# Performance work log

Hardware: AMD Instinct MI355X
Metric: run time of the kernel (lower is better)

Reference implementation:

```python
import jax, jax.numpy as jnp
import numpy as np
from jax.ops import segment_sum

NUM_NODES = 50000
IN_DIM = 512
OUT_DIM = 512
NNZ = 150000
NUM_EDGES = 10000


def setup_inputs() -> dict:
    key = jax.random.key(0)
    k1, k2, k3, k4, k5 = jax.random.split(key, 5)
    X = jax.random.normal(k1, (NUM_NODES, IN_DIM), dtype=jnp.float32)
    V = jax.random.randint(k2, (NNZ,), 0, NUM_NODES)
    E = jax.random.randint(k3, (NNZ,), 0, NUM_EDGES)
    # Linear(in_dim, out_dim) params (torch default init ~ U(-1/sqrt(in), 1/sqrt(in)))
    bound = 1.0 / np.sqrt(IN_DIM)
    W = jax.random.uniform(k4, (OUT_DIM, IN_DIM), minval=-bound, maxval=bound, dtype=jnp.float32)
    b = jax.random.uniform(k5, (OUT_DIM,), minval=-bound, maxval=bound, dtype=jnp.float32)
    eps = jnp.float32(0.1)
    return {"X": X, "V": V, "E": E, "num_edges": NUM_EDGES, "W": W, "b": b, "eps": eps}


def reference(X, V, E, num_edges, W, b, eps):
    num_nodes = X.shape[0]
    # Stage 1: node -> hyperedge (mean of member node features)
    gathered = X[V]  # (nnz, in_dim)
    edge_sum = segment_sum(gathered, E, num_segments=num_edges)          # (num_edges, in_dim)
    count = segment_sum(jnp.ones((E.shape[0],), X.dtype), E, num_segments=num_edges)
    edge_emb = edge_sum / jnp.clip(count, 1.0)[:, None]
    # Stage 2: hyperedge -> node (sum of incident hyperedge embeddings)
    node_msg = segment_sum(edge_emb[E], V, num_segments=num_nodes)       # (num_nodes, in_dim)
    # GIN self-loop + linear
    h = (1.0 + eps) * X + node_msg
    return h @ W.T + b
```

## Files before the change

kernel.cpp:

```cpp
#include <hip/hip_runtime.h>

#define D     512
#define NEDGE 10000
#define ECAP  48
#define NCAP  24
#define CPAD  32

typedef __attribute__((ext_vector_type(8))) short  bf16x8;
typedef __attribute__((ext_vector_type(4))) float  f32x4;
typedef __attribute__((ext_vector_type(8))) unsigned short u16x8;

static __device__ __forceinline__ unsigned short f2bf(float f) {
    union { float f; unsigned u; } c; c.f = f;
    unsigned u = c.u;
    return (unsigned short)((u + 0x7FFFu + ((u >> 16) & 1u)) >> 16);
}
static __device__ __forceinline__ float bf2f(unsigned short s) {
    union { unsigned u; float f; } c; c.u = ((unsigned)s) << 16; return c.f;
}

__global__ __launch_bounds__(256)
void prep(const int* __restrict__ V, const int* __restrict__ E,
          const float* __restrict__ W, const float* __restrict__ X,
          int* __restrict__ ecnt, int* __restrict__ ncnt,
          int* __restrict__ emem, int* __restrict__ nmem,
          unsigned short* __restrict__ wb, unsigned short* __restrict__ xb,
          int nnz, int xgroups)
{
    const int i = blockIdx.x * 256 + threadIdx.x;
    if (i < nnz) {
        const int e = E[i], v = V[i];
        const int p = atomicAdd(&ecnt[(size_t)e * CPAD], 1);
        if (p < ECAP) emem[e * ECAP + p] = v;
        const int q = atomicAdd(&ncnt[(size_t)v * CPAD], 1);
        if (q < NCAP) nmem[v * NCAP + q] = e;
    }
    if (i < xgroups) {
        const float4 a = *(reinterpret_cast<const float4*>(X) + i);
        ushort4 o;
        o.x = f2bf(a.x); o.y = f2bf(a.y); o.z = f2bf(a.z); o.w = f2bf(a.w);
        *(reinterpret_cast<ushort4*>(xb) + i) = o;
    }
    if (i < D * D / 4) {
        const float4 a = *(reinterpret_cast<const float4*>(W) + i);
        ushort4 o;
        o.x = f2bf(a.x); o.y = f2bf(a.y); o.z = f2bf(a.z); o.w = f2bf(a.w);
        *(reinterpret_cast<ushort4*>(wb) + i) = o;
    }
}

__global__ __launch_bounds__(256, 5)
void gemm_y(const unsigned short* __restrict__ xb, const unsigned short* __restrict__ wb,
            unsigned short* __restrict__ y, int M, int q, int r)
{
    __shared__ unsigned short S[2 * 128 * 64];
    unsigned short* As = S;
    unsigned short* Bs = S + 128 * 64;

    const int orig = blockIdx.x;
    const int xcd = orig & 7, lin = orig >> 3;
    const int wg = (xcd < r ? xcd * (q + 1) : r * (q + 1) + (xcd - r) * q) + lin;
    const int row0 = (wg >> 2) * 128;
    const int col0 = (wg & 3) * 128;

    const int tid  = threadIdx.x;
    const int lane = tid & 63;
    const int wave = tid >> 6;
    const int wr = wave >> 1, wc = wave & 1;

    const int l15   = lane & 15;
    const int khalf = lane >> 4;
    const int crow  = lane >> 3;
    const int slot  = lane & 7;

    f32x4 acc[4][4] = {};

    for (int t = 0; t < 8; ++t) {
        const int k0 = t * 64;
        #pragma unroll
        for (int cc = 0; cc < 8; ++cc) {
            const int chunk = wave * 8 + cc;
            const unsigned short* src; unsigned short* dst; int c, base;
            if (chunk < 16) { c = chunk;      src = xb; base = row0; dst = As; }
            else            { c = chunk - 16; src = wb; base = col0; dst = Bs; }
            const int rr = c * 8 + crow;
            const int gslot = slot ^ (rr & 7);
            const unsigned short* gp = src + (size_t)(base + rr) * D + k0 + gslot * 8;
            unsigned short* lp = dst + c * 512;
            __builtin_amdgcn_global_load_lds(
                (const __attribute__((address_space(1))) void*)gp,
                (__attribute__((address_space(3))) void*)lp, 16, 0, 0);
        }
        asm volatile("s_waitcnt vmcnt(0)" ::: "memory");
        __syncthreads();

        #pragma unroll
        for (int s = 0; s < 2; ++s) {
            bf16x8 a[4], b[4];
            #pragma unroll
            for (int i = 0; i < 4; ++i) {
                const int rr = wr * 64 + i * 16 + l15;
                const int sl = (khalf | (s << 2)) ^ (rr & 7);
                a[i] = *reinterpret_cast<const bf16x8*>(As + rr * 64 + sl * 8);
            }
            #pragma unroll
            for (int j = 0; j < 4; ++j) {
                const int rr = wc * 64 + j * 16 + l15;
                const int sl = (khalf | (s << 2)) ^ (rr & 7);
                b[j] = *reinterpret_cast<const bf16x8*>(Bs + rr * 64 + sl * 8);
            }
            #pragma unroll
            for (int i = 0; i < 4; ++i)
                #pragma unroll
                for (int j = 0; j < 4; ++j)
                    acc[i][j] = __builtin_amdgcn_mfma_f32_16x16x32_bf16(a[i], b[j], acc[i][j], 0, 0, 0);
        }
        __syncthreads();
    }

    const int row4 = (lane >> 4) * 4;
    #pragma unroll
    for (int j = 0; j < 4; ++j) {
        const int lc = wc * 64 + j * 16 + l15;
        #pragma unroll
        for (int i = 0; i < 4; ++i) {
            #pragma unroll
            for (int reg = 0; reg < 4; ++reg) {
                const int lr = wr * 64 + i * 16 + row4 + reg;
                const float own = acc[i][j][reg];
                const float nb  = __shfl_xor(own, 1);
                if (!(lane & 1)) {
                    const unsigned dw = (unsigned)f2bf(own) | ((unsigned)f2bf(nb) << 16);
                    *reinterpret_cast<unsigned*>(S + lr * 128 + lc) = dw;
                }
            }
        }
    }
    __syncthreads();
    #pragma unroll
    for (int k = 0; k < 8; ++k) {
        const int lr  = k * 16 + (tid >> 4);
        const int lc8 = (tid & 15) * 8;
        const int gr  = row0 + lr;
        if (gr < M) {
            const u16x8 vv = *reinterpret_cast<const u16x8*>(S + lr * 128 + lc8);
            *reinterpret_cast<u16x8*>(y + (size_t)gr * D + col0 + lc8) = vv;
        }
    }
}

__global__ __launch_bounds__(256)
void edge_gather(const unsigned short* __restrict__ y, const int* __restrict__ ecnt,
                 const int* __restrict__ emem, unsigned short* __restrict__ ey)
{
    __shared__ float red[D];
    const int e = blockIdx.x;
    const int t = threadIdx.x;
    const int half = t >> 7;
    const int l = t & 127;
    int deg = ecnt[(size_t)e * CPAD]; if (deg > ECAP) deg = ECAP;
    const int* lst = emem + e * ECAP;
    float4 acc = make_float4(0.f, 0.f, 0.f, 0.f);
    for (int m = half; m < deg; m += 2) {
        const int v = lst[m];
        const ushort4 x = *reinterpret_cast<const ushort4*>(y + (size_t)v * D + l * 4);
        acc.x += bf2f(x.x); acc.y += bf2f(x.y);
        acc.z += bf2f(x.z); acc.w += bf2f(x.w);
    }
    if (half) *reinterpret_cast<float4*>(red + l * 4) = acc;
    __syncthreads();
    if (!half) {
        const float4 o = *reinterpret_cast<const float4*>(red + l * 4);
        const float inv = 1.0f / fmaxf((float)deg, 1.0f);
        ushort4 r;
        r.x = f2bf((acc.x + o.x) * inv);
        r.y = f2bf((acc.y + o.y) * inv);
        r.z = f2bf((acc.z + o.z) * inv);
        r.w = f2bf((acc.w + o.w) * inv);
        *reinterpret_cast<ushort4*>(ey + (size_t)e * D + l * 4) = r;
    }
}

__global__ __launch_bounds__(128)
void build_out(const unsigned short* __restrict__ y, const unsigned short* __restrict__ ey,
               const int* __restrict__ ncnt, const int* __restrict__ nmem,
               const float* __restrict__ eps_p, const float* __restrict__ bias,
               float* __restrict__ out, int M)
{
    const int v = blockIdx.x;
    if (v >= M) return;
    const int t = threadIdx.x;
    const float scale = 1.0f + *eps_p;
    const ushort4 yv = *reinterpret_cast<const ushort4*>(y + (size_t)v * D + t * 4);
    const float4 bv = *reinterpret_cast<const float4*>(bias + t * 4);
    float4 acc;
    acc.x = scale * bf2f(yv.x) + bv.x;
    acc.y = scale * bf2f(yv.y) + bv.y;
    acc.z = scale * bf2f(yv.z) + bv.z;
    acc.w = scale * bf2f(yv.w) + bv.w;
    int deg = ncnt[(size_t)v * CPAD]; if (deg > NCAP) deg = NCAP;
    const int* lst = nmem + v * NCAP;
    for (int m = 0; m < deg; ++m) {
        const int e = lst[m];
        const ushort4 g = *reinterpret_cast<const ushort4*>(ey + (size_t)e * D + t * 4);
        acc.x += bf2f(g.x); acc.y += bf2f(g.y);
        acc.z += bf2f(g.z); acc.w += bf2f(g.w);
    }
    *reinterpret_cast<float4*>(out + (size_t)v * D + t * 4) = acc;
}

extern "C" void kernel_launch(void* const* d_in, const int* in_sizes, int n_in,
                              void* d_out, int out_size, void* d_ws, size_t ws_size,
                              hipStream_t stream)
{
    const float* X    = (const float*)d_in[0];
    const int*   V    = (const int*)  d_in[1];
    const int*   E    = (const int*)  d_in[2];
    const float* W    = (const float*)d_in[4];
    const float* bias = (const float*)d_in[5];
    const float* eps  = (const float*)d_in[6];
    float* out = (float*)d_out;

    const int nnz = in_sizes[1];
    const int M   = in_sizes[0] / D;
    const int Mpad = ((M + 127) / 128) * 128;

    char* w = (char*)d_ws;
    int* ecnt = (int*)w;
    int* ncnt = ecnt + (size_t)NEDGE * CPAD;
    size_t off = ((size_t)NEDGE + M) * CPAD * sizeof(int);
    int* emem = (int*)(w + off);            off += (size_t)NEDGE * ECAP * sizeof(int);
    int* nmem = (int*)(w + off);            off += (size_t)M * NCAP * sizeof(int);
    off = (off + 255) & ~(size_t)255;
    unsigned short* xbuf = (unsigned short*)(w + off);
    unsigned short* eybf = xbuf;
    off += (size_t)M * D * sizeof(unsigned short);
    unsigned short* ybuf = (unsigned short*)(w + off); off += (size_t)Mpad * D * sizeof(unsigned short);
    unsigned short* wbuf = (unsigned short*)(w + off); off += (size_t)D * D * sizeof(unsigned short);

    hipMemsetAsync(ecnt, 0, ((size_t)NEDGE + M) * CPAD * sizeof(int), stream);

    const int xgroups = M * D / 4;
    prep<<<(xgroups + 255) / 256, 256, 0, stream>>>(V, E, W, X, ecnt, ncnt, emem, nmem,
                                                    wbuf, xbuf, nnz, xgroups);

    const int nwg = (Mpad / 128) * (D / 128);
    gemm_y<<<nwg, 256, 0, stream>>>(xbuf, wbuf, ybuf, M, nwg / 8, nwg % 8);

    edge_gather<<<NEDGE, 256, 0, stream>>>(ybuf, ecnt, emem, eybf);
    build_out  <<<M, 128, 0, stream>>>(ybuf, eybf, ncnt, nmem, eps, bias, out, M);
}
```

Baseline: 177.0 us.

## Fuse fp32-to-bf16 conversion of X into GEMM A-tile load

Drops the separate pass that converted X to a bf16 buffer. The GEMM now reads fp32 X directly, converts it in registers and writes swizzled bf16 into LDS, which removes a full write and re-read of a bf16 copy of X. The counter padding stride also shrinks from 32 to 8 ints, cutting memset size. The trade-off is that A-tile loads become synchronous register loads instead of async global-to-LDS transfers, and the GEMM reads twice as many bytes for A, repeated for each of the four column tiles.

```diff
diff --git a/kernel.cpp b/kernel.cpp
--- a/kernel.cpp
+++ b/kernel.cpp
@@ -4,7 +4,7 @@
 #define NEDGE 10000
 #define ECAP  48
 #define NCAP  24
-#define CPAD  32
+#define CPAD  8
 
 typedef __attribute__((ext_vector_type(8))) short  bf16x8;
 typedef __attribute__((ext_vector_type(4))) float  f32x4;
@@ -21,11 +21,10 @@
 
 __global__ __launch_bounds__(256)
 void prep(const int* __restrict__ V, const int* __restrict__ E,
-          const float* __restrict__ W, const float* __restrict__ X,
+          const float* __restrict__ W,
           int* __restrict__ ecnt, int* __restrict__ ncnt,
           int* __restrict__ emem, int* __restrict__ nmem,
-          unsigned short* __restrict__ wb, unsigned short* __restrict__ xb,
-          int nnz, int xgroups)
+          unsigned short* __restrict__ wb, int nnz)
 {
     const int i = blockIdx.x * 256 + threadIdx.x;
     if (i < nnz) {
@@ -35,12 +34,6 @@
         const int q = atomicAdd(&ncnt[(size_t)v * CPAD], 1);
         if (q < NCAP) nmem[v * NCAP + q] = e;
     }
-    if (i < xgroups) {
-        const float4 a = *(reinterpret_cast<const float4*>(X) + i);
-        ushort4 o;
-        o.x = f2bf(a.x); o.y = f2bf(a.y); o.z = f2bf(a.z); o.w = f2bf(a.w);
-        *(reinterpret_cast<ushort4*>(xb) + i) = o;
-    }
     if (i < D * D / 4) {
         const float4 a = *(reinterpret_cast<const float4*>(W) + i);
         ushort4 o;
@@ -50,7 +43,7 @@
 }
 
 __global__ __launch_bounds__(256, 5)
-void gemm_y(const unsigned short* __restrict__ xb, const unsigned short* __restrict__ wb,
+void gemm_y(const float* __restrict__ X, const unsigned short* __restrict__ wb,
             unsigned short* __restrict__ y, int M, int q, int r)
 {
     __shared__ unsigned short S[2 * 128 * 64];
@@ -73,23 +66,41 @@
     const int crow  = lane >> 3;
     const int slot  = lane & 7;
 
+    const int arow  = tid & 127;
+    const int ahalf = tid >> 7;
+    int grA = row0 + arow; if (grA >= M) grA = M - 1;
+    const float* xrow = X + (size_t)grA * D + ahalf * 32;
+    unsigned short* awr = As + arow * 64;
+    const int aswz = arow & 7;
+
     f32x4 acc[4][4] = {};
 
     for (int t = 0; t < 8; ++t) {
         const int k0 = t * 64;
         #pragma unroll
-        for (int cc = 0; cc < 8; ++cc) {
-            const int chunk = wave * 8 + cc;
-            const unsigned short* src; unsigned short* dst; int c, base;
-            if (chunk < 16) { c = chunk;      src = xb; base = row0; dst = As; }
-            else            { c = chunk - 16; src = wb; base = col0; dst = Bs; }
+        for (int cc = 0; cc < 4; ++cc) {
+            const int c = wave * 4 + cc;
             const int rr = c * 8 + crow;
             const int gslot = slot ^ (rr & 7);
-            const unsigned short* gp = src + (size_t)(base + rr) * D + k0 + gslot * 8;
-            unsigned short* lp = dst + c * 512;
+            const unsigned short* gp = wb + (size_t)(col0 + rr) * D + k0 + gslot * 8;
+            unsigned short* lp = Bs + c * 512;
             __builtin_amdgcn_global_load_lds(
                 (const __attribute__((address_space(1))) void*)gp,
                 (__attribute__((address_space(3))) void*)lp, 16, 0, 0);
+        }
+        float4 av[8];
+        #pragma unroll
+        for (int u = 0; u < 8; ++u)
+            av[u] = *reinterpret_cast<const float4*>(xrow + k0 + u * 4);
+        #pragma unroll
+        for (int u = 0; u < 4; ++u) {
+            u16x8 o;
+            o[0] = f2bf(av[2*u].x);   o[1] = f2bf(av[2*u].y);
+            o[2] = f2bf(av[2*u].z);   o[3] = f2bf(av[2*u].w);
+            o[4] = f2bf(av[2*u+1].x); o[5] = f2bf(av[2*u+1].y);
+            o[6] = f2bf(av[2*u+1].z); o[7] = f2bf(av[2*u+1].w);
+            const int s = ahalf * 4 + u;
+            *reinterpret_cast<u16x8*>(awr + (s ^ aswz) * 8) = o;
         }
         asm volatile("s_waitcnt vmcnt(0)" ::: "memory");
         __syncthreads();
@@ -232,20 +243,16 @@
     int* emem = (int*)(w + off);            off += (size_t)NEDGE * ECAP * sizeof(int);
     int* nmem = (int*)(w + off);            off += (size_t)M * NCAP * sizeof(int);
     off = (off + 255) & ~(size_t)255;
-    unsigned short* xbuf = (unsigned short*)(w + off);
-    unsigned short* eybf = xbuf;
-    off += (size_t)M * D * sizeof(unsigned short);
     unsigned short* ybuf = (unsigned short*)(w + off); off += (size_t)Mpad * D * sizeof(unsigned short);
+    unsigned short* eybf = (unsigned short*)(w + off); off += (size_t)NEDGE * D * sizeof(unsigned short);
     unsigned short* wbuf = (unsigned short*)(w + off); off += (size_t)D * D * sizeof(unsigned short);
 
     hipMemsetAsync(ecnt, 0, ((size_t)NEDGE + M) * CPAD * sizeof(int), stream);
 
-    const int xgroups = M * D / 4;
-    prep<<<(xgroups + 255) / 256, 256, 0, stream>>>(V, E, W, X, ecnt, ncnt, emem, nmem,
-                                                    wbuf, xbuf, nnz, xgroups);
+    prep<<<(nnz + 255) / 256, 256, 0, stream>>>(V, E, W, ecnt, ncnt, emem, nmem, wbuf, nnz);
 
     const int nwg = (Mpad / 128) * (D / 128);
-    gemm_y<<<nwg, 256, 0, stream>>>(xbuf, wbuf, ybuf, M, nwg / 8, nwg % 8);
+    gemm_y<<<nwg, 256, 0, stream>>>(X, wbuf, ybuf, M, nwg / 8, nwg % 8);
 
     edge_gather<<<NEDGE, 256, 0, stream>>>(ybuf, ecnt, emem, eybf);
     build_out  <<<M, 128, 0, stream>>>(ybuf, eybf, ncnt, nmem, eps, bias, out, M);
```

Result: slower. 328.0 us (+85.3%).
